# Kernel tuning notes

Hardware: AMD Instinct MI355X
Metric: run time of the kernel (lower is better)

The kernel has to match this reference:

```python
import jax, jax.numpy as jnp
import numpy as np

N_CUI, N_CODE, D = 100_000, 50_000, 128
F, L = 2, 2  # graph_num_filters, graph_num_layers
E_CC, E_KC, E_CK = 1_600_000, 800_000, 800_000


def setup_inputs() -> dict:
    key = jax.random.key(0)
    ks = jax.random.split(key, 11)
    x_cui = jax.random.normal(ks[0], (N_CUI, D), jnp.float32)
    x_code = jax.random.normal(ks[1], (N_CODE, D), jnp.float32)
    # edge_index tensors: row 0 = src, row 1 = dst
    ei_cc = jnp.stack([jax.random.randint(ks[2], (E_CC,), 0, N_CUI),
                       jax.random.randint(ks[3], (E_CC,), 0, N_CUI)])
    ei_kc = jnp.stack([jax.random.randint(ks[4], (E_KC,), 0, N_CODE),
                       jax.random.randint(ks[5], (E_KC,), 0, N_CUI)])
    ei_ck = jnp.stack([jax.random.randint(ks[6], (E_CK,), 0, N_CUI),
                       jax.random.randint(ks[7], (E_CK,), 0, N_CODE)])
    scale = 1.0 / np.sqrt(D)
    # [filter, layer, edge_type, D, D]; edge_type 0: cui->cui, 1: code->cui, 2: cui->code
    Wl = jax.random.normal(ks[8], (F, L, 3, D, D), jnp.float32) * scale
    Wr = jax.random.normal(ks[9], (F, L, 3, D, D), jnp.float32) * scale
    b = jax.random.normal(ks[10], (F, L, 3, D), jnp.float32) * 0.01
    return {"x_cui": x_cui, "x_code": x_code, "ei_cc": ei_cc, "ei_kc": ei_kc,
            "ei_ck": ei_ck, "Wl": Wl, "Wr": Wr, "b": b}


def _sage(x_src, x_dst, ei, Wl, Wr, b):
    """PyG SAGEConv(aggr='mean', normalize=False): lin_l(mean_msg) + lin_r(x_dst)."""
    n_dst = x_dst.shape[0]
    msg = x_src[ei[0]]  # [E, D] gather
    agg = jax.ops.segment_sum(msg, ei[1], num_segments=n_dst)  # [n_dst, D]
    cnt = jax.ops.segment_sum(jnp.ones((ei.shape[1],), msg.dtype), ei[1],
                              num_segments=n_dst)
    mean = agg / jnp.maximum(cnt, 1.0)[:, None]  # zero in-degree -> 0 (as PyG)
    return mean @ Wl.T + b + x_dst @ Wr.T


def reference(x_cui, x_code, ei_cc, ei_kc, ei_ck, Wl, Wr, b):
    outs_cui, outs_code = [], []
    for f in range(F):
        h_cui, h_code = x_cui, x_code
        for l in range(L):
            # HeteroConv aggr='sum': sum conv outputs per destination node type
            o_cui = (_sage(h_cui, h_cui, ei_cc, Wl[f, l, 0], Wr[f, l, 0], b[f, l, 0])
                     + _sage(h_code, h_cui, ei_kc, Wl[f, l, 1], Wr[f, l, 1], b[f, l, 1]))
            o_code = _sage(h_cui, h_code, ei_ck, Wl[f, l, 2], Wr[f, l, 2], b[f, l, 2])
            if l < L - 1:  # relu between layers only
                o_cui, o_code = jax.nn.relu(o_cui), jax.nn.relu(o_code)
            h_cui, h_code = o_cui, o_code
        outs_cui.append(h_cui)
        outs_code.append(h_code)
    # max over filter stacks
    out_cui = jnp.max(jnp.stack(outs_cui), axis=0)
    out_code = jnp.max(jnp.stack(outs_code), axis=0)
    return out_cui, out_code
```

## Files before the change

### kernel.cpp

```cpp
#include <hip/hip_runtime.h>

typedef unsigned short ushortT;
typedef __attribute__((ext_vector_type(8))) short short8v;
typedef __attribute__((ext_vector_type(4))) float float4v;

constexpr int D = 128;

__device__ __forceinline__ void splitf(float v, short& h, short& l) {
    unsigned u = __float_as_uint(v);
    unsigned hb = u & 0xffff0000u;
    float r = v - __uint_as_float(hb);
    h = (short)(u >> 16);
    l = (short)(__float_as_uint(r) >> 16);
}
__device__ __forceinline__ unsigned packsplit(float v) {
    unsigned u = __float_as_uint(v);
    unsigned hb = u & 0xffff0000u;
    float r = v - __uint_as_float(hb);
    return hb | (__float_as_uint(r) >> 16);
}
__device__ __forceinline__ float unpackf(unsigned p) {
    return __uint_as_float(p & 0xffff0000u) + __uint_as_float(p << 16);
}

__global__ void count_all(const int* __restrict__ ecc, const int* __restrict__ ekc,
                          const int* __restrict__ eck, int Ecc, int Ekc, int Eck,
                          int ncui, int* __restrict__ cnt) {
    int ET = Ecc + Ekc + Eck;
    for (int e = blockIdx.x * blockDim.x + threadIdx.x; e < ET;
         e += gridDim.x * blockDim.x) {
        int d;
        if (e < Ecc)            d = ecc[Ecc + e];
        else if (e < Ecc + Ekc) d = ncui + ekc[Ekc + (e - Ecc)];
        else                    d = 2 * ncui + eck[Eck + (e - Ecc - Ekc)];
        atomicAdd(&cnt[d], 1);
    }
}

__global__ void place_all(const int* __restrict__ ecc, const int* __restrict__ ekc,
                          const int* __restrict__ eck, int Ecc, int Ekc, int Eck,
                          int ncui, int* __restrict__ cur, int* __restrict__ csr) {
    int ET = Ecc + Ekc + Eck;
    for (int e = blockIdx.x * blockDim.x + threadIdx.x; e < ET;
         e += gridDim.x * blockDim.x) {
        int d, s;
        if (e < Ecc)            { s = ecc[e]; d = ecc[Ecc + e]; }
        else if (e < Ecc + Ekc) { int le = e - Ecc; s = ekc[le]; d = ncui + ekc[Ekc + le]; }
        else                    { int le = e - Ecc - Ekc; s = eck[le]; d = 2 * ncui + eck[Eck + le]; }
        int p = atomicAdd(&cur[d], 1);
        csr[p] = s;
    }
}

__global__ __launch_bounds__(1024) void scan_s1(const int* __restrict__ cnt, int n4,
                                                int* __restrict__ blockSums) {
    __shared__ int red[1024];
    int t = threadIdx.x;
    int i = blockIdx.x * 1024 + t;
    int4 v = (i < n4) ? ((const int4*)cnt)[i] : make_int4(0, 0, 0, 0);
    red[t] = v.x + v.y + v.z + v.w;
    __syncthreads();
    for (int s = 512; s > 0; s >>= 1) {
        if (t < s) red[t] += red[t + s];
        __syncthreads();
    }
    if (t == 0) blockSums[blockIdx.x] = red[0];
}

__global__ __launch_bounds__(1024) void scan_s2(int* __restrict__ bs, int nb,
                                                int* __restrict__ offs, int NT) {
    __shared__ int s[1024];
    int t = threadIdx.x;
    int v = (t < nb) ? bs[t] : 0;
    s[t] = v;
    __syncthreads();
    for (int d = 1; d < 1024; d <<= 1) {
        int u = (t >= d) ? s[t - d] : 0;
        __syncthreads();
        s[t] += u;
        __syncthreads();
    }
    if (t < nb) bs[t] = s[t] - v;
    if (t == 0) offs[NT] = s[1023];
}

__global__ __launch_bounds__(1024) void scan_s3(const int* __restrict__ cnt, int n,
                                                const int* __restrict__ blockSums,
                                                int* __restrict__ offs, int* __restrict__ cur,
                                                float* __restrict__ inv) {
    __shared__ int sc[1024];
    int t = threadIdx.x;
    int n4 = n >> 2;
    int i4 = blockIdx.x * 1024 + t;
    int4 v = (i4 < n4) ? ((const int4*)cnt)[i4] : make_int4(0, 0, 0, 0);
    int s1 = v.x, s2 = s1 + v.y, s3 = s2 + v.z, s4 = s3 + v.w;
    sc[t] = s4;
    __syncthreads();
    for (int d = 1; d < 1024; d <<= 1) {
        int u = (t >= d) ? sc[t - d] : 0;
        __syncthreads();
        sc[t] += u;
        __syncthreads();
    }
    int base = sc[t] - s4 + blockSums[blockIdx.x];
    if (i4 < n4) {
        int4 o;
        o.x = base; o.y = base + s1; o.z = base + s2; o.w = base + s3;
        ((int4*)offs)[i4] = o;
        ((int4*)cur)[i4]  = o;
        float4 iv;
        iv.x = 1.f / fmaxf((float)v.x, 1.f);
        iv.y = 1.f / fmaxf((float)v.y, 1.f);
        iv.z = 1.f / fmaxf((float)v.z, 1.f);
        iv.w = 1.f / fmaxf((float)v.w, 1.f);
        ((float4*)inv)[i4] = iv;
    }
}

__global__ void prep_w(const float* __restrict__ Wl, const float* __restrict__ Wr,
                       const float* __restrict__ b, ushortT* __restrict__ Wp,
                       float* __restrict__ bcomb) {
    if (blockIdx.x == 160) {
        for (int t = threadIdx.x; t < 512; t += 256) {
            int fl = t >> 7, c = t & 127;
            bcomb[t] = b[(fl * 3 + 0) * D + c] + b[(fl * 3 + 1) * D + c];
        }
        return;
    }
    int id = blockIdx.x * 256 + threadIdx.x;
    int mat = id >> 11;
    int slot = id & 2047;
    int nt = slot >> 8, rem = slot & 255, ks = rem >> 6, lane = rem & 63;
    int row = nt * 16 + (lane & 15);
    int k0 = ks * 32 + ((lane >> 4) << 3);
    int fl = mat / 5, j = mat % 5;
    const float* s1;
    const float* s2 = nullptr;
    if (j < 2)       s1 = Wl + (size_t)(fl * 3 + j) * D * D;
    else if (j == 2) { s1 = Wr + (size_t)(fl * 3 + 0) * D * D;
                       s2 = Wr + (size_t)(fl * 3 + 1) * D * D; }
    else if (j == 3) s1 = Wl + (size_t)(fl * 3 + 2) * D * D;
    else             s1 = Wr + (size_t)(fl * 3 + 2) * D * D;

    unsigned hw[4], lw[4];
    #pragma unroll
    for (int q = 0; q < 4; ++q) {
        short h0, l0, h1, l1;
        float v0 = s1[row * D + k0 + 2 * q];
        float v1 = s1[row * D + k0 + 2 * q + 1];
        if (s2) { v0 += s2[row * D + k0 + 2 * q]; v1 += s2[row * D + k0 + 2 * q + 1]; }
        splitf(v0, h0, l0);
        splitf(v1, h1, l1);
        hw[q] = (unsigned short)h0 | ((unsigned)(unsigned short)h1 << 16);
        lw[q] = (unsigned short)l0 | ((unsigned)(unsigned short)l1 << 16);
    }
    ushortT* dh = Wp + (size_t)mat * 32768 + slot * 8;
    *(uint4*)dh           = make_uint4(hw[0], hw[1], hw[2], hw[3]);
    *(uint4*)(dh + 16384) = make_uint4(lw[0], lw[1], lw[2], lw[3]);
}

__global__ void agg_all(const float* __restrict__ src_cui_f, const float* __restrict__ src_code_f,
                        const unsigned* __restrict__ src_cui_p, const unsigned* __restrict__ src_code_p,
                        int packed, const int* __restrict__ csr, const int* __restrict__ offs,
                        const float* __restrict__ inv, int ncui, int ncode,
                        unsigned* __restrict__ outP) {
    int NT = 2 * ncui + ncode;
    int gw = (int)((blockIdx.x * (size_t)blockDim.x + threadIdx.x) >> 6);
    int lane = threadIdx.x & 63;
    if (gw >= NT) return;
    bool isCode = (gw >= ncui) && (gw < 2 * ncui);
    int st = offs[gw], en = offs[gw + 1];
    float a0 = 0, a1 = 0, b0 = 0, b1 = 0, c0 = 0, c1 = 0, d0 = 0, d1 = 0;
    int e = st;
    if (!packed) {
        const float* s = isCode ? src_code_f : src_cui_f;
        for (; e + 4 <= en; e += 4) {
            int i0 = csr[e], i1 = csr[e + 1], i2 = csr[e + 2], i3 = csr[e + 3];
            float2 q0 = ((const float2*)(s + (size_t)i0 * D))[lane];
            float2 q1 = ((const float2*)(s + (size_t)i1 * D))[lane];
            float2 q2 = ((const float2*)(s + (size_t)i2 * D))[lane];
            float2 q3 = ((const float2*)(s + (size_t)i3 * D))[lane];
            a0 += q0.x; a1 += q0.y; b0 += q1.x; b1 += q1.y;
            c0 += q2.x; c1 += q2.y; d0 += q3.x; d1 += q3.y;
        }
        for (; e < en; ++e) {
            float2 q = ((const float2*)(s + (size_t)csr[e] * D))[lane];
            a0 += q.x; a1 += q.y;
        }
    } else {
        const unsigned* s = isCode ? src_code_p : src_cui_p;
        for (; e + 4 <= en; e += 4) {
            int i0 = csr[e], i1 = csr[e + 1], i2 = csr[e + 2], i3 = csr[e + 3];
            uint2 q0 = ((const uint2*)(s + (size_t)i0 * D))[lane];
            uint2 q1 = ((const uint2*)(s + (size_t)i1 * D))[lane];
            uint2 q2 = ((const uint2*)(s + (size_t)i2 * D))[lane];
            uint2 q3 = ((const uint2*)(s + (size_t)i3 * D))[lane];
            a0 += unpackf(q0.x); a1 += unpackf(q0.y);
            b0 += unpackf(q1.x); b1 += unpackf(q1.y);
            c0 += unpackf(q2.x); c1 += unpackf(q2.y);
            d0 += unpackf(q3.x); d1 += unpackf(q3.y);
        }
        for (; e < en; ++e) {
            uint2 q = ((const uint2*)(s + (size_t)csr[e] * D))[lane];
            a0 += unpackf(q.x); a1 += unpackf(q.y);
        }
    }
    float sc = inv[gw];
    float r0 = ((a0 + b0) + (c0 + d0)) * sc;
    float r1 = ((a1 + b1) + (c1 + d1)) * sc;
    ((uint2*)(outP + (size_t)gw * D))[lane] = make_uint2(packsplit(r0), packsplit(r1));
}

__global__ __launch_bounds__(256, 2) void gemm_split(
    const unsigned* __restrict__ A0, const unsigned* __restrict__ A1,
    const unsigned* __restrict__ A2, const float* __restrict__ Alast_f32,
    const ushortT* __restrict__ W0, const ushortT* __restrict__ W1,
    const ushortT* __restrict__ W2, const float* __restrict__ bias,
    float* __restrict__ outF, unsigned* __restrict__ outP,
    int M, int nPairs, int mode) {
    __shared__ ushortT wlds[32768];

    int tid = threadIdx.x;
    int lane = tid & 63;
    int w = tid >> 6;
    int rowTile = blockIdx.x * 256 + w * 64;
    int rl = lane & 15;
    int kg = (lane >> 4) << 3;

    float4v acc[4][8];
    #pragma unroll
    for (int mt = 0; mt < 4; ++mt)
        #pragma unroll
        for (int nt = 0; nt < 8; ++nt)
            acc[mt][nt] = (float4v){0.f, 0.f, 0.f, 0.f};

    const unsigned* Aarr[3] = {A0, A1, A2};
    const ushortT* Warr[3] = {W0, W1, W2};

    for (int p = 0; p < nPairs; ++p) {
        __syncthreads();
        {
            const ushortT* Wsrc = Warr[p];
            #pragma unroll
            for (int i = 0; i < 16; ++i)
                *(int4*)&wlds[i * 2048 + tid * 8] = *(const int4*)&Wsrc[i * 2048 + tid * 8];
        }
        __syncthreads();
        bool f32A = (Alast_f32 != nullptr) && (p == nPairs - 1);
        const unsigned* A = Aarr[p];
        #pragma unroll
        for (int ks = 0; ks < 4; ++ks) {
            short8v ah[4], al[4];
            #pragma unroll
            for (int mt = 0; mt < 4; ++mt) {
                int row = rowTile + mt * 16 + rl;
                if (row < M) {
                    size_t boff = (size_t)row * D + ks * 32 + kg;
                    if (!f32A) {
                        uint4 q0 = *(const uint4*)(A + boff);
                        uint4 q1 = *(const uint4*)(A + boff + 4);
                        unsigned qa[8] = {q0.x, q0.y, q0.z, q0.w, q1.x, q1.y, q1.z, q1.w};
                        #pragma unroll
                        for (int jj = 0; jj < 8; ++jj) {
                            ah[mt][jj] = (short)(qa[jj] >> 16);
                            al[mt][jj] = (short)(qa[jj] & 0xffffu);
                        }
                    } else {
                        float4 f0 = *(const float4*)(Alast_f32 + boff);
                        float4 f1 = *(const float4*)(Alast_f32 + boff + 4);
                        float fa[8] = {f0.x, f0.y, f0.z, f0.w, f1.x, f1.y, f1.z, f1.w};
                        #pragma unroll
                        for (int jj = 0; jj < 8; ++jj) {
                            short hh, ll;
                            splitf(fa[jj], hh, ll);
                            ah[mt][jj] = hh;
                            al[mt][jj] = ll;
                        }
                    }
                } else {
                    #pragma unroll
                    for (int jj = 0; jj < 8; ++jj) { ah[mt][jj] = 0; al[mt][jj] = 0; }
                }
            }
            #pragma unroll
            for (int nt = 0; nt < 8; ++nt) {
                short8v bh = *(const short8v*)&wlds[nt * 2048 + ks * 512 + lane * 8];
                short8v bl = *(const short8v*)&wlds[16384 + nt * 2048 + ks * 512 + lane * 8];
                #pragma unroll
                for (int mt = 0; mt < 4; ++mt)
                    acc[mt][nt] = __builtin_amdgcn_mfma_f32_16x16x32_bf16(ah[mt], bh, acc[mt][nt], 0, 0, 0);
                #pragma unroll
                for (int mt = 0; mt < 4; ++mt)
                    acc[mt][nt] = __builtin_amdgcn_mfma_f32_16x16x32_bf16(ah[mt], bl, acc[mt][nt], 0, 0, 0);
                #pragma unroll
                for (int mt = 0; mt < 4; ++mt)
                    acc[mt][nt] = __builtin_amdgcn_mfma_f32_16x16x32_bf16(al[mt], bh, acc[mt][nt], 0, 0, 0);
            }
        }
    }

    #pragma unroll
    for (int nt = 0; nt < 8; ++nt) {
        int col = nt * 16 + rl;
        float bv = bias[col];
        #pragma unroll
        for (int mt = 0; mt < 4; ++mt) {
            int r0 = rowTile + mt * 16 + ((lane >> 4) << 2);
            float4v c = acc[mt][nt];
            #pragma unroll
            for (int r = 0; r < 4; ++r) {
                int row = r0 + r;
                if (row >= M) continue;
                float v = c[r] + bv;
                if (mode == 0) {
                    v = fmaxf(v, 0.f);
                    outP[(size_t)row * D + col] = packsplit(v);
                } else if (mode == 1) {
                    outF[(size_t)row * D + col] = v;
                } else {
                    float* pp = outF + (size_t)row * D + col;
                    *pp = fmaxf(*pp, v);
                }
            }
        }
    }
}

extern "C" void kernel_launch(void* const* d_in, const int* in_sizes, int n_in,
                              void* d_out, int out_size, void* d_ws, size_t ws_size,
                              hipStream_t stream) {
    const float* x_cui  = (const float*)d_in[0];
    const float* x_code = (const float*)d_in[1];
    const int*   ei_cc  = (const int*)d_in[2];
    const int*   ei_kc  = (const int*)d_in[3];
    const int*   ei_ck  = (const int*)d_in[4];
    const float* Wl     = (const float*)d_in[5];
    const float* Wr     = (const float*)d_in[6];
    const float* b      = (const float*)d_in[7];

    const int N_CUI  = in_sizes[0] / D;
    const int N_CODE = in_sizes[1] / D;
    const int E_CC   = in_sizes[2] / 2;
    const int E_KC   = in_sizes[3] / 2;
    const int E_CK   = in_sizes[4] / 2;
    const int NT = 2 * N_CUI + N_CODE;
    const int ET = E_CC + E_KC + E_CK;

    char* ws = (char*)d_ws;
    size_t off = 0;
    auto alloc = [&](size_t bytes) -> char* {
        char* p = ws + off;
        off += (bytes + 255) & ~(size_t)255;
        return p;
    };

    int*      cntAll    = (int*)alloc((size_t)NT * 4);
    size_t cntBytes = (size_t)NT * 4;
    int*      offsAll   = (int*)alloc(((size_t)NT + 4) * 4);
    int*      curAll    = (int*)alloc((size_t)NT * 4);
    float*    invAll    = (float*)alloc((size_t)NT * 4);
    int*      blockSums = (int*)alloc(1024 * 4);
    int*      csrAll    = (int*)alloc((size_t)ET * 4);
    ushortT*  Wp        = (ushortT*)alloc((size_t)20 * 32768 * 2);
    float*    bcomb     = (float*)alloc(512 * 4);
    unsigned* aggP      = (unsigned*)alloc((size_t)NT * D * 4);
    unsigned* hcuiP0    = (unsigned*)alloc((size_t)N_CUI * D * 4);
    unsigned* hcuiP1    = (unsigned*)alloc((size_t)N_CUI * D * 4);
    unsigned* hcodeP0   = (unsigned*)alloc((size_t)N_CODE * D * 4);
    unsigned* hcodeP1   = (unsigned*)alloc((size_t)N_CODE * D * 4);

    float* out_cui  = (float*)d_out;
    float* out_code = (float*)d_out + (size_t)N_CUI * D;

    unsigned* hcP[2] = {hcuiP0, hcuiP1};
    unsigned* hkP[2] = {hcodeP0, hcodeP1};

    const unsigned* aggCC = aggP;
    const unsigned* aggKC = aggP + (size_t)N_CUI * D;
    const unsigned* aggCK = aggP + (size_t)2 * N_CUI * D;

    hipMemsetAsync(d_ws, 0, cntBytes, stream);
    count_all<<<2048, 256, 0, stream>>>(ei_cc, ei_kc, ei_ck, E_CC, E_KC, E_CK, N_CUI, cntAll);
    int n4 = NT >> 2;
    int nb = (n4 + 1023) / 1024;
    scan_s1<<<nb, 1024, 0, stream>>>(cntAll, n4, blockSums);
    scan_s2<<<1, 1024, 0, stream>>>(blockSums, nb, offsAll, NT);
    scan_s3<<<nb, 1024, 0, stream>>>(cntAll, NT, blockSums, offsAll, curAll, invAll);
    place_all<<<2048, 256, 0, stream>>>(ei_cc, ei_kc, ei_ck, E_CC, E_KC, E_CK, N_CUI, curAll, csrAll);
    prep_w<<<161, 256, 0, stream>>>(Wl, Wr, b, Wp, bcomb);

    int aggGrid = (NT + 3) / 4;
    int gCui = (N_CUI + 255) / 256;
    int gCode = (N_CODE + 255) / 256;
    auto WpM = [&](int m) { return (const ushortT*)(Wp + (size_t)m * 32768); };

    agg_all<<<aggGrid, 256, 0, stream>>>(x_cui, x_code, nullptr, nullptr, 0,
                                         csrAll, offsAll, invAll, N_CUI, N_CODE, aggP);
    for (int f = 0; f < 2; ++f) {
        int fl = f * 2;
        gemm_split<<<gCui, 256, 0, stream>>>(
            aggCC, aggKC, aggCC , x_cui,
            WpM(fl * 5 + 0), WpM(fl * 5 + 1), WpM(fl * 5 + 2),
            bcomb + fl * D, nullptr, hcP[f], N_CUI, 3, 0);
    }
    for (int f = 0; f < 2; ++f) {
        int fl = f * 2;
        gemm_split<<<gCode, 256, 0, stream>>>(
            aggCK, aggCK , aggCK , x_code,
            WpM(fl * 5 + 3), WpM(fl * 5 + 4), WpM(fl * 5 + 4),
            b + (size_t)(fl * 3 + 2) * D, nullptr, hkP[f], N_CODE, 2, 0);
    }

    for (int f = 0; f < 2; ++f) {
        int fl = f * 2 + 1;
        int mode = (f == 0) ? 1 : 2;
        agg_all<<<aggGrid, 256, 0, stream>>>(nullptr, nullptr, hcP[f], hkP[f], 1,
                                             csrAll, offsAll, invAll, N_CUI, N_CODE, aggP);
        gemm_split<<<gCui, 256, 0, stream>>>(
            aggCC, aggKC, hcP[f], nullptr,
            WpM(fl * 5 + 0), WpM(fl * 5 + 1), WpM(fl * 5 + 2),
            bcomb + fl * D, out_cui, nullptr, N_CUI, 3, mode);
        gemm_split<<<gCode, 256, 0, stream>>>(
            aggCK, hkP[f], hkP[f] , nullptr,
            WpM(fl * 5 + 3), WpM(fl * 5 + 4), WpM(fl * 5 + 4),
            b + (size_t)(fl * 3 + 2) * D, out_code, nullptr, N_CODE, 2, mode);
    }
}
```

Baseline: 1.852 ms.

## Bucket edges by destination block before CSR placement; widen gather unroll

CSR construction now bins each edge into a coarse destination bucket of 256 nodes during the counting pass. A per-bucket placement kernel then scatters edges within that bucket, so the scatter writes into csr stay localized instead of random across the whole array. Edges beyond the bucket capacity go to an overflow list that a separate kernel places. The aggregation kernel also unrolls its gather to 8 independent row loads with separate accumulators to raise memory-level parallelism, which adds register pressure and changes the float summation order.

```diff
diff --git a/kernel.cpp b/kernel.cpp
--- a/kernel.cpp
+++ b/kernel.cpp
@@ -5,6 +5,8 @@
 typedef __attribute__((ext_vector_type(4))) float float4v;
 
 constexpr int D = 128;
+constexpr int BKT_CAP = 8192;
+constexpr int OVF_CAP = 1 << 20;
 
 __device__ __forceinline__ void splitf(float v, short& h, short& l) {
     unsigned u = __float_as_uint(v);
@@ -23,23 +25,11 @@
     return __uint_as_float(p & 0xffff0000u) + __uint_as_float(p << 16);
 }
 
-__global__ void count_all(const int* __restrict__ ecc, const int* __restrict__ ekc,
-                          const int* __restrict__ eck, int Ecc, int Ekc, int Eck,
-                          int ncui, int* __restrict__ cnt) {
-    int ET = Ecc + Ekc + Eck;
-    for (int e = blockIdx.x * blockDim.x + threadIdx.x; e < ET;
-         e += gridDim.x * blockDim.x) {
-        int d;
-        if (e < Ecc)            d = ecc[Ecc + e];
-        else if (e < Ecc + Ekc) d = ncui + ekc[Ekc + (e - Ecc)];
-        else                    d = 2 * ncui + eck[Eck + (e - Ecc - Ekc)];
-        atomicAdd(&cnt[d], 1);
-    }
-}
-
-__global__ void place_all(const int* __restrict__ ecc, const int* __restrict__ ekc,
-                          const int* __restrict__ eck, int Ecc, int Ekc, int Eck,
-                          int ncui, int* __restrict__ cur, int* __restrict__ csr) {
+__global__ void bucket_count(const int* __restrict__ ecc, const int* __restrict__ ekc,
+                             const int* __restrict__ eck, int Ecc, int Ekc, int Eck,
+                             int ncui, int* __restrict__ cnt, int* __restrict__ bktCur,
+                             unsigned* __restrict__ bkt, int* __restrict__ ovfCnt,
+                             int* __restrict__ ovf) {
     int ET = Ecc + Ekc + Eck;
     for (int e = blockIdx.x * blockDim.x + threadIdx.x; e < ET;
          e += gridDim.x * blockDim.x) {
@@ -47,6 +37,40 @@
         if (e < Ecc)            { s = ecc[e]; d = ecc[Ecc + e]; }
         else if (e < Ecc + Ekc) { int le = e - Ecc; s = ekc[le]; d = ncui + ekc[Ekc + le]; }
         else                    { int le = e - Ecc - Ekc; s = eck[le]; d = 2 * ncui + eck[Eck + le]; }
+        atomicAdd(&cnt[d], 1);
+        int b = d >> 8;
+        int p = atomicAdd(&bktCur[b * 16], 1);
+        if (p < BKT_CAP) {
+            bkt[(size_t)b * BKT_CAP + p] = ((unsigned)(d & 255) << 24) | (unsigned)s;
+        } else {
+            int q = atomicAdd(ovfCnt, 1);
+            if (q < OVF_CAP) { ovf[q * 2] = s; ovf[q * 2 + 1] = d; }
+        }
+    }
+}
+
+__global__ void bucket_place(const unsigned* __restrict__ bkt, const int* __restrict__ bktCur,
+                             int* __restrict__ cur, int* __restrict__ csr) {
+    int b = blockIdx.x;
+    int n = bktCur[b * 16];
+    if (n > BKT_CAP) n = BKT_CAP;
+    int base = b << 8;
+    for (int t = threadIdx.x; t < n; t += blockDim.x) {
+        unsigned e = bkt[(size_t)b * BKT_CAP + t];
+        int s = (int)(e & 0xFFFFFFu);
+        int d = base + (int)(e >> 24);
+        int p = atomicAdd(&cur[d], 1);
+        csr[p] = s;
+    }
+}
+
+__global__ void place_ovf(const int* __restrict__ ovfCnt, const int* __restrict__ ovf,
+                          int* __restrict__ cur, int* __restrict__ csr) {
+    int n = *ovfCnt;
+    if (n > OVF_CAP) n = OVF_CAP;
+    for (int i = blockIdx.x * blockDim.x + threadIdx.x; i < n;
+         i += gridDim.x * blockDim.x) {
+        int s = ovf[i * 2], d = ovf[i * 2 + 1];
         int p = atomicAdd(&cur[d], 1);
         csr[p] = s;
     }
@@ -170,44 +194,66 @@
     if (gw >= NT) return;
     bool isCode = (gw >= ncui) && (gw < 2 * ncui);
     int st = offs[gw], en = offs[gw + 1];
-    float a0 = 0, a1 = 0, b0 = 0, b1 = 0, c0 = 0, c1 = 0, d0 = 0, d1 = 0;
+    float ax[8], ay[8];
+    #pragma unroll
+    for (int j = 0; j < 8; ++j) { ax[j] = 0.f; ay[j] = 0.f; }
     int e = st;
     if (!packed) {
         const float* s = isCode ? src_code_f : src_cui_f;
+        for (; e + 8 <= en; e += 8) {
+            int idx[8];
+            #pragma unroll
+            for (int j = 0; j < 8; ++j) idx[j] = csr[e + j];
+            #pragma unroll
+            for (int j = 0; j < 8; ++j) {
+                float2 q = ((const float2*)(s + (size_t)idx[j] * D))[lane];
+                ax[j] += q.x; ay[j] += q.y;
+            }
+        }
         for (; e + 4 <= en; e += 4) {
-            int i0 = csr[e], i1 = csr[e + 1], i2 = csr[e + 2], i3 = csr[e + 3];
-            float2 q0 = ((const float2*)(s + (size_t)i0 * D))[lane];
-            float2 q1 = ((const float2*)(s + (size_t)i1 * D))[lane];
-            float2 q2 = ((const float2*)(s + (size_t)i2 * D))[lane];
-            float2 q3 = ((const float2*)(s + (size_t)i3 * D))[lane];
-            a0 += q0.x; a1 += q0.y; b0 += q1.x; b1 += q1.y;
-            c0 += q2.x; c1 += q2.y; d0 += q3.x; d1 += q3.y;
+            int idx[4];
+            #pragma unroll
+            for (int j = 0; j < 4; ++j) idx[j] = csr[e + j];
+            #pragma unroll
+            for (int j = 0; j < 4; ++j) {
+                float2 q = ((const float2*)(s + (size_t)idx[j] * D))[lane];
+                ax[j] += q.x; ay[j] += q.y;
+            }
         }
         for (; e < en; ++e) {
             float2 q = ((const float2*)(s + (size_t)csr[e] * D))[lane];
-            a0 += q.x; a1 += q.y;
+            ax[0] += q.x; ay[0] += q.y;
         }
     } else {
         const unsigned* s = isCode ? src_code_p : src_cui_p;
+        for (; e + 8 <= en; e += 8) {
+            int idx[8];
+            #pragma unroll
+            for (int j = 0; j < 8; ++j) idx[j] = csr[e + j];
+            #pragma unroll
+            for (int j = 0; j < 8; ++j) {
+                uint2 q = ((const uint2*)(s + (size_t)idx[j] * D))[lane];
+                ax[j] += unpackf(q.x); ay[j] += unpackf(q.y);
+            }
+        }
         for (; e + 4 <= en; e += 4) {
-            int i0 = csr[e], i1 = csr[e + 1], i2 = csr[e + 2], i3 = csr[e + 3];
-            uint2 q0 = ((const uint2*)(s + (size_t)i0 * D))[lane];
-            uint2 q1 = ((const uint2*)(s + (size_t)i1 * D))[lane];
-            uint2 q2 = ((const uint2*)(s + (size_t)i2 * D))[lane];
-            uint2 q3 = ((const uint2*)(s + (size_t)i3 * D))[lane];
-            a0 += unpackf(q0.x); a1 += unpackf(q0.y);
-            b0 += unpackf(q1.x); b1 += unpackf(q1.y);
-            c0 += unpackf(q2.x); c1 += unpackf(q2.y);
-            d0 += unpackf(q3.x); d1 += unpackf(q3.y);
+            int idx[4];
+            #pragma unroll
+            for (int j = 0; j < 4; ++j) idx[j] = csr[e + j];
+            #pragma unroll
+            for (int j = 0; j < 4; ++j) {
+                uint2 q = ((const uint2*)(s + (size_t)idx[j] * D))[lane];
+                ax[j] += unpackf(q.x); ay[j] += unpackf(q.y);
+            }
         }
         for (; e < en; ++e) {
             uint2 q = ((const uint2*)(s + (size_t)csr[e] * D))[lane];
-            a0 += unpackf(q.x); a1 += unpackf(q.y);
+            ax[0] += unpackf(q.x); ay[0] += unpackf(q.y);
         }
     }
     float sc = inv[gw];
-    float r0 = ((a0 + b0) + (c0 + d0)) * sc;
-    float r1 = ((a1 + b1) + (c1 + d1)) * sc;
+    float r0 = (((ax[0] + ax[1]) + (ax[2] + ax[3])) + ((ax[4] + ax[5]) + (ax[6] + ax[7]))) * sc;
+    float r1 = (((ay[0] + ay[1]) + (ay[2] + ay[3])) + ((ay[4] + ay[5]) + (ay[6] + ay[7]))) * sc;
     ((uint2*)(outP + (size_t)gw * D))[lane] = make_uint2(packsplit(r0), packsplit(r1));
 }
 
@@ -345,6 +391,7 @@
     const int E_CK   = in_sizes[4] / 2;
     const int NT = 2 * N_CUI + N_CODE;
     const int ET = E_CC + E_KC + E_CK;
+    const int NB = (NT + 255) >> 8;
 
     char* ws = (char*)d_ws;
     size_t off = 0;
@@ -355,7 +402,10 @@
     };
 
     int*      cntAll    = (int*)alloc((size_t)NT * 4);
-    size_t cntBytes = (size_t)NT * 4;
+    int*      bktCur    = (int*)alloc((size_t)NB * 16 * 4);
+    int*      ovfCnt    = (int*)alloc(64);
+    size_t cntBytes = off;
+
     int*      offsAll   = (int*)alloc(((size_t)NT + 4) * 4);
     int*      curAll    = (int*)alloc((size_t)NT * 4);
     float*    invAll    = (float*)alloc((size_t)NT * 4);
@@ -369,6 +419,9 @@
     unsigned* hcodeP0   = (unsigned*)alloc((size_t)N_CODE * D * 4);
     unsigned* hcodeP1   = (unsigned*)alloc((size_t)N_CODE * D * 4);
 
+    unsigned* bkt = aggP;
+    int*      ovf = (int*)(aggP + (size_t)NB * BKT_CAP);
+
     float* out_cui  = (float*)d_out;
     float* out_code = (float*)d_out + (size_t)N_CUI * D;
 
@@ -380,13 +433,15 @@
     const unsigned* aggCK = aggP + (size_t)2 * N_CUI * D;
 
     hipMemsetAsync(d_ws, 0, cntBytes, stream);
-    count_all<<<2048, 256, 0, stream>>>(ei_cc, ei_kc, ei_ck, E_CC, E_KC, E_CK, N_CUI, cntAll);
+    bucket_count<<<2048, 256, 0, stream>>>(ei_cc, ei_kc, ei_ck, E_CC, E_KC, E_CK,
+                                           N_CUI, cntAll, bktCur, bkt, ovfCnt, ovf);
     int n4 = NT >> 2;
     int nb = (n4 + 1023) / 1024;
     scan_s1<<<nb, 1024, 0, stream>>>(cntAll, n4, blockSums);
     scan_s2<<<1, 1024, 0, stream>>>(blockSums, nb, offsAll, NT);
     scan_s3<<<nb, 1024, 0, stream>>>(cntAll, NT, blockSums, offsAll, curAll, invAll);
-    place_all<<<2048, 256, 0, stream>>>(ei_cc, ei_kc, ei_ck, E_CC, E_KC, E_CK, N_CUI, curAll, csrAll);
+    bucket_place<<<NB, 256, 0, stream>>>(bkt, bktCur, curAll, csrAll);
+    place_ovf<<<64, 256, 0, stream>>>(ovfCnt, ovf, curAll, csrAll);
     prep_w<<<161, 256, 0, stream>>>(Wl, Wr, b, Wp, bcomb);
 
     int aggGrid = (NT + 3) / 4;
```

After: 1.882 ms. No clear change (+1.6%).
